# Optimization experiments

Measured on AMD Instinct MI355X. Metric: run time of the kernel, lower is better.

Reference implementation:

```python
import jax, jax.numpy as jnp
import numpy as np

N = 12288
E = 393216
IN_DIM = 128
HID = 64
QK = 32
K_HOPS = 2


def setup_inputs() -> dict:
    key = jax.random.key(0)
    ks = jax.random.split(key, 12)
    s = lambda k, shp, fan: jax.random.normal(k, shp, jnp.float32) / np.sqrt(fan)
    return {
        "x_train": jax.random.normal(ks[0], (N, IN_DIM), jnp.float32),
        "x_ori": jax.random.normal(ks[1], (N, IN_DIM), jnp.float32),
        "edge_index": jax.random.randint(ks[2], (2, E), 0, N, jnp.int64),
        "mask": jnp.zeros((N,), jnp.bool_),
        "W1": s(ks[3], (IN_DIM, HID), IN_DIM), "b1": jnp.zeros((HID,), jnp.float32),
        "W2": s(ks[4], (HID, HID), HID),      "b2": jnp.zeros((HID,), jnp.float32),
        "Wq": s(ks[5], (HID, QK), HID),       "bq": jnp.zeros((QK,), jnp.float32),
        "Wk": s(ks[6], (HID, QK), HID),       "bk": jnp.zeros((QK,), jnp.float32),
        "Wv": s(ks[7], (HID, HID), HID),      "bv": jnp.zeros((HID,), jnp.float32),
        "Wdx": s(ks[8], (HID, IN_DIM), HID),  "bdx": jnp.zeros((IN_DIM,), jnp.float32),
    }


def reference(x_train, x_ori, edge_index, mask,
              W1, b1, W2, b2, Wq, bq, Wk, bk, Wv, bv, Wdx, bdx):
    n = x_train.shape[0]
    row, col = edge_index[0], edge_index[1]

    # shared MLP: linear -> relu -> linear2 -> relu
    enc = lambda x: jax.nn.relu(jax.nn.relu(x @ W1 + b1) @ W2 + b2)
    h_ori = enc(x_ori)      # [N, HID]
    h_train = enc(x_train)  # [N, HID]

    # degree of source nodes, D^{-1/2}
    deg = jax.ops.segment_sum(jnp.ones_like(row, jnp.float32), row, num_segments=n)
    d_invsqrt = jnp.clip(deg, 1.0, None) ** -0.5  # [N]
    d_invsqrt = d_invsqrt[:, None]

    def lap(x):
        h = x * d_invsqrt
        out = jax.ops.segment_sum(h[row], col, num_segments=n)
        return x - out * d_invsqrt

    a_feat = 2.0 * h_train - lap(h_train)  # low-pass: 2I - L_sym
    stack = [a_feat]
    x = h_train
    for _ in range(K_HOPS):  # dropout inert in eval mode
        x = lap(x)
        stack.append(x)
    L = jnp.stack(stack, axis=1)  # [N, K+1, HID]

    # attention with global mean-pooled query over h_ori[~mask]
    w = (~mask).astype(jnp.float32)
    q_nodes = h_ori @ Wq + bq                              # [N, QK]
    q_global = (q_nodes * w[:, None]).sum(0) / jnp.clip(w.sum(), 1.0, None)  # [QK]
    keys = L @ Wk + bk   # [N, K+1, QK]
    vals = L @ Wv + bv   # [N, K+1, HID]
    scale = 1.0 / np.sqrt(HID)  # scale uses D = keys feature dim BEFORE projection
    scores = jnp.einsum('q,nkq->nk', q_global, keys) * scale
    A = jax.nn.softmax(scores, axis=-1)          # [N, K+1]
    z = jnp.einsum('nk,nkd->nd', A, vals)        # [N, HID]

    x_hat = z @ Wdx + bdx   # [N, IN_DIM]
    adj_hat = z @ z.T       # [N, N]
    return x_hat, adj_hat
```

## Files before the change

kernel.cpp:

```cpp
#include <hip/hip_runtime.h>
#include <hip/hip_bf16.h>

constexpr int N_  = 12288;
constexpr int E_  = 393216;
constexpr int IND = 128;
constexpr int HID = 64;
constexpr int QKD = 32;
constexpr int CAP = 96;

typedef __attribute__((ext_vector_type(4))) float f4raw;
typedef __attribute__((ext_vector_type(8))) __bf16 bf16x8;
typedef __attribute__((ext_vector_type(4))) __bf16 bf16x4;
typedef __attribute__((ext_vector_type(16))) float f32x16;

__device__ inline bf16x8 lds_read_bf8(const char* base, int row, int k) {
  int off = (row * 128 + k * 2) ^ ((row & 7) << 4);
  uint4 u = *(const uint4*)(base + off);
  union { uint4 u; bf16x8 v; } c; c.u = u; return c.v;
}
__device__ inline void lds_write_bf(char* base, int row, int col, __bf16 v) {
  int off = (row * 128 + col * 2) ^ ((row & 7) << 4);
  *(__bf16*)(base + off) = v;
}

__global__ __launch_bounds__(256) void prep_graph_kernel(
    const int* __restrict__ row, const int* __restrict__ col,
    const float* __restrict__ W1, const float* __restrict__ W2,
    const float* __restrict__ Wv, const float* __restrict__ Wdx,
    __bf16* __restrict__ W1T, __bf16* __restrict__ W2T,
    __bf16* __restrict__ WvT, __bf16* __restrict__ WdxT,
    int* degRow, int* cntCol, int* __restrict__ csrRow) {
  int b = blockIdx.x, tid = threadIdx.x;
  if (b < 384) {
    int e0 = (b * 256 + tid) * 4;
    int4 r4 = *(const int4*)(row + e0);
    atomicAdd(&degRow[r4.x], 1);
    atomicAdd(&degRow[r4.y], 1);
    atomicAdd(&degRow[r4.z], 1);
    atomicAdd(&degRow[r4.w], 1);
  } else if (b < 768) {
    int e0 = ((b - 384) * 256 + tid) * 4;
    int4 r4 = *(const int4*)(row + e0);
    int4 c4 = *(const int4*)(col + e0);
    int p;
    p = atomicAdd(&cntCol[c4.x], 1); csrRow[c4.x * CAP + p] = r4.x;
    p = atomicAdd(&cntCol[c4.y], 1); csrRow[c4.y * CAP + p] = r4.y;
    p = atomicAdd(&cntCol[c4.z], 1); csrRow[c4.z * CAP + p] = r4.z;
    p = atomicAdd(&cntCol[c4.w], 1); csrRow[c4.w * CAP + p] = r4.w;
  } else if (b == 768) {
    for (int e = tid; e < IND * HID; e += 256) {
      int c = e >> 7, k = e & 127;
      W1T[e] = (__bf16)W1[k * HID + c];
    }
  } else if (b == 769) {
    for (int e = tid; e < HID * HID; e += 256) {
      int c = e >> 6, k = e & 63;
      W2T[e] = (__bf16)W2[k * HID + c];
    }
  } else if (b == 770) {
    for (int e = tid; e < HID * HID; e += 256) {
      int c = e >> 6, k = e & 63;
      WvT[e] = (__bf16)Wv[k * HID + c];
    }
  } else {
    for (int e = tid; e < HID * IND; e += 256) {
      int c = e >> 6, k = e & 63;
      WdxT[e] = (__bf16)Wdx[k * IND + c];
    }
  }
}

__global__ __launch_bounds__(256) void enc_dinv_kernel(
    const float* __restrict__ xo, const float* __restrict__ xt,
    const __bf16* __restrict__ W1T, const float* __restrict__ b1,
    const __bf16* __restrict__ W2T, const float* __restrict__ b2,
    const int* __restrict__ degRow, const unsigned char* __restrict__ mask,
    float* __restrict__ h_tr, float* __restrict__ dinv, float* __restrict__ gsum) {
  __shared__ __align__(16) char h1s[2][32 * 128];
  __shared__ float wls[64];
  int b = blockIdx.x, tid = threadIdx.x;
  if (b >= 384) {
    int i0 = ((b - 384) * 256 + tid) * 4;
    int4 dg = *(const int4*)(degRow + i0);
    f4raw o = {rsqrtf((float)max(dg.x, 1)), rsqrtf((float)max(dg.y, 1)),
               rsqrtf((float)max(dg.z, 1)), rsqrtf((float)max(dg.w, 1))};
    *(f4raw*)(dinv + i0) = o;
    return;
  }
  bool ori = b < 192;
  int row0 = (ori ? b : b - 192) * 64;
  const float* xrow = (ori ? xo : xt) + (size_t)row0 * IND;
  if (ori && tid < 64) wls[tid] = mask[row0 + tid] ? 0.f : 1.f;
  int wave = tid >> 6, lane = tid & 63;
  int p = wave >> 1, w2 = wave & 1;
  int lr = lane & 31, hi = lane >> 5;
  int colc = w2 * 32 + lr;
  f32x16 acc = (f32x16)(0.f);
  const __bf16* wcol = W1T + (size_t)colc * IND + hi * 8;
  const float* arow = xrow + (size_t)(p * 32 + lr) * IND + hi * 8;
#pragma unroll
  for (int kk = 0; kk < 8; ++kk) {
    f4raw v0 = *(const f4raw*)(arow + kk * 16);
    f4raw v1 = *(const f4raw*)(arow + kk * 16 + 4);
    bf16x8 a;
    a[0] = (__bf16)v0.x; a[1] = (__bf16)v0.y; a[2] = (__bf16)v0.z; a[3] = (__bf16)v0.w;
    a[4] = (__bf16)v1.x; a[5] = (__bf16)v1.y; a[6] = (__bf16)v1.z; a[7] = (__bf16)v1.w;
    bf16x8 bq = *(const bf16x8*)(wcol + kk * 16);
    acc = __builtin_amdgcn_mfma_f32_32x32x16_bf16(a, bq, acc, 0, 0, 0);
  }
  float b1l = b1[colc];
#pragma unroll
  for (int reg = 0; reg < 16; ++reg) {
    int rr = (reg & 3) + 8 * (reg >> 2) + 4 * hi;
    float v = fmaxf(acc[reg] + b1l, 0.f);
    lds_write_bf(h1s[p], rr, colc, (__bf16)v);
  }
  __syncthreads();
  f32x16 acc2 = (f32x16)(0.f);
  const __bf16* wcol2 = W2T + (size_t)colc * HID + hi * 8;
#pragma unroll
  for (int kk = 0; kk < 4; ++kk) {
    bf16x8 a = lds_read_bf8(h1s[p], lr, kk * 16 + hi * 8);
    bf16x8 bq = *(const bf16x8*)(wcol2 + kk * 16);
    acc2 = __builtin_amdgcn_mfma_f32_32x32x16_bf16(a, bq, acc2, 0, 0, 0);
  }
  float b2l = b2[colc];
  if (ori) {
    float part = 0.f;
#pragma unroll
    for (int reg = 0; reg < 16; ++reg) {
      int rr = (reg & 3) + 8 * (reg >> 2) + 4 * hi;
      float v = fmaxf(acc2[reg] + b2l, 0.f);
      part = fmaf(wls[p * 32 + rr], v, part);
    }
    atomicAdd(&gsum[colc], part);
    if (tid == 0) {
      float wl = 0.f;
      for (int r = 0; r < 64; ++r) wl += wls[r];
      atomicAdd(&gsum[64], wl);
    }
  } else {
#pragma unroll
    for (int reg = 0; reg < 16; ++reg) {
      int rr = (reg & 3) + 8 * (reg >> 2) + 4 * hi;
      float v = fmaxf(acc2[reg] + b2l, 0.f);
      h_tr[(size_t)(row0 + p * 32 + rr) * HID + colc] = v;
    }
  }
}

__global__ __launch_bounds__(256) void lap1_kernel(
    const float* __restrict__ h, const float* __restrict__ dinv,
    const int* __restrict__ cnt, const int* __restrict__ csrRow,
    float* __restrict__ lap1d) {
  int lane = threadIdx.x & 63, wv = threadIdx.x >> 6;
  int g = lane >> 4, t = lane & 15;
  int c = blockIdx.x * 16 + wv * 4 + g;
  int s0 = c * CAP, s1 = s0 + cnt[c];
  f4raw a0 = (f4raw)(0.f), a1 = (f4raw)(0.f), a2 = (f4raw)(0.f), a3 = (f4raw)(0.f);
  int i = s0;
  for (; i + 3 < s1; i += 4) {
    int r0 = csrRow[i], r1 = csrRow[i + 1], r2 = csrRow[i + 2], r3 = csrRow[i + 3];
    a0 += (*(const f4raw*)(h + (size_t)r0 * HID + t * 4)) * dinv[r0];
    a1 += (*(const f4raw*)(h + (size_t)r1 * HID + t * 4)) * dinv[r1];
    a2 += (*(const f4raw*)(h + (size_t)r2 * HID + t * 4)) * dinv[r2];
    a3 += (*(const f4raw*)(h + (size_t)r3 * HID + t * 4)) * dinv[r3];
  }
  for (; i < s1; ++i) {
    int r0 = csrRow[i];
    a0 += (*(const f4raw*)(h + (size_t)r0 * HID + t * 4)) * dinv[r0];
  }
  float d = dinv[c];
  size_t idx = (size_t)c * HID + t * 4;
  f4raw hc = *(const f4raw*)(h + idx);
  *(f4raw*)(lap1d + idx) = (hc - ((a0 + a1) + (a2 + a3)) * d) * d;
}

__global__ __launch_bounds__(256) void lap2_attnz_xhat_kernel(
    const float* __restrict__ h, const float* __restrict__ lap1d,
    const float* __restrict__ dinv,
    const int* __restrict__ cnt, const int* __restrict__ csrRow,
    const float* __restrict__ gsum,
    const float* __restrict__ Wq, const float* __restrict__ bq,
    const float* __restrict__ Wk, const float* __restrict__ bk,
    const __bf16* __restrict__ WvT, const float* __restrict__ bv,
    const __bf16* __restrict__ WdxT, const float* __restrict__ bdx,
    float* __restrict__ xhat, __bf16* __restrict__ zb) {
  __shared__ float l2s[32][68];
  __shared__ __align__(16) char zps[32 * 128];
  __shared__ __align__(16) char zsl[32 * 128];
  __shared__ float qg[QKD];
  __shared__ float kqs[72];
  int tid = threadIdx.x;
  int row0 = blockIdx.x * 32;
  float wsum = gsum[64];
  if (tid < QKD) {
    float inv = 1.0f / fmaxf(wsum, 1.0f);
    float a = bq[tid] * wsum;
    for (int d0 = 0; d0 < HID; ++d0) a = fmaf(gsum[d0], Wq[d0 * QKD + tid], a);
    qg[tid] = a * inv;
  }
  int grp = tid >> 4, t = tid & 15;
#pragma unroll
  for (int it = 0; it < 2; ++it) {
    int r = grp + 16 * it;
    int c = row0 + r;
    int s0 = c * CAP, s1 = s0 + cnt[c];
    f4raw a0 = (f4raw)(0.f), a1 = (f4raw)(0.f), a2 = (f4raw)(0.f), a3 = (f4raw)(0.f);
    int i = s0;
    for (; i + 3 < s1; i += 4) {
      int r0 = csrRow[i], r1 = csrRow[i + 1], r2 = csrRow[i + 2], r3 = csrRow[i + 3];
      a0 += *(const f4raw*)(lap1d + (size_t)r0 * HID + t * 4);
      a1 += *(const f4raw*)(lap1d + (size_t)r1 * HID + t * 4);
      a2 += *(const f4raw*)(lap1d + (size_t)r2 * HID + t * 4);
      a3 += *(const f4raw*)(lap1d + (size_t)r3 * HID + t * 4);
    }
    for (; i < s1; ++i) {
      int r0 = csrRow[i];
      a0 += *(const f4raw*)(lap1d + (size_t)r0 * HID + t * 4);
    }
    float d = dinv[c];
    float rd = 1.0f / d;
    f4raw lv = *(const f4raw*)(lap1d + (size_t)c * HID + t * 4);
    *(f4raw*)&l2s[r][t * 4] = lv * rd - ((a0 + a1) + (a2 + a3)) * d;
  }
  __syncthreads();
  if (tid < 64) {
    float a = 0.f;
    for (int q = 0; q < QKD; ++q) a = fmaf(Wk[tid * QKD + q], qg[q], a);
    kqs[tid] = a * 0.125f;
  } else if (tid == 64) {
    float sb = 0.f;
    for (int q = 0; q < QKD; ++q) sb = fmaf(bk[q], qg[q], sb);
    kqs[64] = sb * 0.125f;
  }
  __syncthreads();
  f4raw kq4 = *(const f4raw*)(&kqs[t * 4]);
  float sbias = kqs[64];
#pragma unroll
  for (int it = 0; it < 2; ++it) {
    int r = grp + 16 * it;
    int c = row0 + r;
    size_t idx = (size_t)c * HID + t * 4;
    float d = dinv[c];
    float rd = 1.0f / d;
    f4raw hv = *(const f4raw*)(h + idx);
    f4raw v1 = *(const f4raw*)(lap1d + idx) * rd;
    f4raw v2 = *(const f4raw*)&l2s[r][t * 4];
    f4raw av = 2.f * hv - v1;
    float s0 = av.x * kq4.x + av.y * kq4.y + av.z * kq4.z + av.w * kq4.w;
    float s1 = v1.x * kq4.x + v1.y * kq4.y + v1.z * kq4.z + v1.w * kq4.w;
    float s2 = v2.x * kq4.x + v2.y * kq4.y + v2.z * kq4.z + v2.w * kq4.w;
#pragma unroll
    for (int o = 1; o < 16; o <<= 1) {
      s0 += __shfl_xor(s0, o);
      s1 += __shfl_xor(s1, o);
      s2 += __shfl_xor(s2, o);
    }
    s0 += sbias; s1 += sbias; s2 += sbias;
    float m = fmaxf(s0, fmaxf(s1, s2));
    float e0 = __expf(s0 - m), e1 = __expf(s1 - m), e2 = __expf(s2 - m);
    float is = 1.f / (e0 + e1 + e2);
    f4raw zp = (e0 * av + e1 * v1 + e2 * v2) * is;
    bf16x4 z4;
    z4[0] = (__bf16)zp.x; z4[1] = (__bf16)zp.y; z4[2] = (__bf16)zp.z; z4[3] = (__bf16)zp.w;
    int off = (r * 128 + t * 8) ^ ((r & 7) << 4);
    *(bf16x4*)(zps + off) = z4;
  }
  __syncthreads();
  int wave = tid >> 6, lane = tid & 63;
  int lr = lane & 31, hi = lane >> 5;
  if (wave < 2) {
    int col = wave * 32 + lr;
    f32x16 accz = (f32x16)(0.f);
    const __bf16* wv = WvT + (size_t)col * HID + hi * 8;
#pragma unroll
    for (int kk = 0; kk < 4; ++kk) {
      bf16x8 a = lds_read_bf8(zps, lr, kk * 16 + hi * 8);
      bf16x8 bq = *(const bf16x8*)(wv + kk * 16);
      accz = __builtin_amdgcn_mfma_f32_32x32x16_bf16(a, bq, accz, 0, 0, 0);
    }
    float bvl = bv[col];
#pragma unroll
    for (int reg = 0; reg < 16; ++reg) {
      int rr = (reg & 3) + 8 * (reg >> 2) + 4 * hi;
      __bf16 vb = (__bf16)(accz[reg] + bvl);
      zb[(size_t)(row0 + rr) * HID + col] = vb;
      lds_write_bf(zsl, rr, col, vb);
    }
  }
  __syncthreads();
  {
    int c0 = wave * 32 + lr;
    f32x16 acx = (f32x16)(0.f);
    const __bf16* wd = WdxT + (size_t)c0 * HID + hi * 8;
#pragma unroll
    for (int kk = 0; kk < 4; ++kk) {
      bf16x8 a = lds_read_bf8(zsl, lr, kk * 16 + hi * 8);
      bf16x8 bq = *(const bf16x8*)(wd + kk * 16);
      acx = __builtin_amdgcn_mfma_f32_32x32x16_bf16(a, bq, acx, 0, 0, 0);
    }
    float bdl = bdx[c0];
#pragma unroll
    for (int reg = 0; reg < 16; ++reg) {
      int rr = (reg & 3) + 8 * (reg >> 2) + 4 * hi;
      xhat[(size_t)(row0 + rr) * IND + c0] = acx[reg] + bdl;
    }
  }
}

__global__ __launch_bounds__(256) void adj_mfma_kernel(
    const __bf16* __restrict__ z, float* __restrict__ out) {
  int tid = threadIdx.x;
  int wave = tid >> 6, lane = tid & 63;
  int wr = wave >> 1, wc = wave & 1;
  int rb = blockIdx.y, cb = blockIdx.x;
  int lr = lane & 31, hi = lane >> 5;

  size_t arow0 = (size_t)(rb * 128 + wr * 64 + lr) * HID;
  size_t arow1 = arow0 + (size_t)32 * HID;
  size_t brow0 = (size_t)(cb * 128 + wc * 64 + lr) * HID;
  size_t brow1 = brow0 + (size_t)32 * HID;
  int kbase = hi * 8;

  f32x16 acc00 = (f32x16)(0.f), acc01 = (f32x16)(0.f);
  f32x16 acc10 = (f32x16)(0.f), acc11 = (f32x16)(0.f);

#pragma unroll
  for (int kk = 0; kk < 4; ++kk) {
    int k0 = kk * 16 + kbase;
    bf16x8 a0 = *(const bf16x8*)(z + arow0 + k0);
    bf16x8 a1 = *(const bf16x8*)(z + arow1 + k0);
    bf16x8 b0 = *(const bf16x8*)(z + brow0 + k0);
    bf16x8 b1 = *(const bf16x8*)(z + brow1 + k0);
    acc00 = __builtin_amdgcn_mfma_f32_32x32x16_bf16(a0, b0, acc00, 0, 0, 0);
    acc01 = __builtin_amdgcn_mfma_f32_32x32x16_bf16(a0, b1, acc01, 0, 0, 0);
    acc10 = __builtin_amdgcn_mfma_f32_32x32x16_bf16(a1, b0, acc10, 0, 0, 0);
    acc11 = __builtin_amdgcn_mfma_f32_32x32x16_bf16(a1, b1, acc11, 0, 0, 0);
  }

  int colb = cb * 128 + wc * 64 + lr;
  int rowb = rb * 128 + wr * 64 + 4 * hi;
#pragma unroll
  for (int reg = 0; reg < 16; ++reg) {
    int rr = (reg & 3) + 8 * (reg >> 2);
    size_t r0 = (size_t)(rowb + rr);
    __builtin_nontemporal_store(acc00[reg], out + r0 * N_ + colb);
    __builtin_nontemporal_store(acc01[reg], out + r0 * N_ + colb + 32);
    __builtin_nontemporal_store(acc10[reg], out + (r0 + 32) * N_ + colb);
    __builtin_nontemporal_store(acc11[reg], out + (r0 + 32) * N_ + colb + 32);
  }
}

extern "C" void kernel_launch(void* const* d_in, const int* in_sizes, int n_in,
                              void* d_out, int out_size, void* d_ws, size_t ws_size,
                              hipStream_t stream) {
  const float* x_train = (const float*)d_in[0];
  const float* x_ori   = (const float*)d_in[1];
  const int*   ei      = (const int*)d_in[2];
  const unsigned char* mask = (const unsigned char*)d_in[3];
  const float* W1  = (const float*)d_in[4];
  const float* b1  = (const float*)d_in[5];
  const float* W2  = (const float*)d_in[6];
  const float* b2  = (const float*)d_in[7];
  const float* Wq  = (const float*)d_in[8];
  const float* bq  = (const float*)d_in[9];
  const float* Wk  = (const float*)d_in[10];
  const float* bk  = (const float*)d_in[11];
  const float* Wv  = (const float*)d_in[12];
  const float* bv  = (const float*)d_in[13];
  const float* Wdx = (const float*)d_in[14];
  const float* bdx = (const float*)d_in[15];

  char* ws = (char*)d_ws;
  size_t o = 0;
  auto alloc = [&](size_t bytes) -> void* {
    void* p = ws + o;
    o += (bytes + 255) & ~(size_t)255;
    return p;
  };
  __bf16* W1T   = (__bf16*)alloc((size_t)IND * HID * 2);
  __bf16* W2T   = (__bf16*)alloc((size_t)HID * HID * 2);
  __bf16* WvT   = (__bf16*)alloc((size_t)HID * HID * 2);
  __bf16* WdxT  = (__bf16*)alloc((size_t)HID * IND * 2);
  float* h_tr   = (float*)alloc((size_t)N_ * HID * 4);
  float* lap1d  = (float*)alloc((size_t)N_ * HID * 4);
  __bf16* zb    = (__bf16*)alloc((size_t)N_ * HID * 2);
  float* dinv   = (float*)alloc((size_t)N_ * 4);
  int*   csrRow = (int*)alloc((size_t)N_ * CAP * 4);
  int*   zero0  = (int*)alloc((size_t)(2 * N_ + 65) * 4);
  int*   degRow = zero0;
  int*   cntCol = zero0 + N_;
  float* gsum   = (float*)(zero0 + 2 * N_);

  const int* row = ei;
  const int* col = ei + E_;

  (void)hipMemsetAsync(zero0, 0, (size_t)(2 * N_ + 65) * 4, stream);

  prep_graph_kernel<<<772, 256, 0, stream>>>(row, col, W1, W2, Wv, Wdx,
                                             W1T, W2T, WvT, WdxT,
                                             degRow, cntCol, csrRow);
  enc_dinv_kernel<<<396, 256, 0, stream>>>(x_ori, x_train, W1T, b1, W2T, b2,
                                           degRow, mask, h_tr, dinv, gsum);
  lap1_kernel<<<N_ / 16, 256, 0, stream>>>(h_tr, dinv, cntCol, csrRow, lap1d);

  float* outp = (float*)d_out;
  lap2_attnz_xhat_kernel<<<N_ / 32, 256, 0, stream>>>(h_tr, lap1d, dinv,
                                                      cntCol, csrRow, gsum,
                                                      Wq, bq, Wk, bk, WvT, bv,
                                                      WdxT, bdx, outp, zb);
  adj_mfma_kernel<<<dim3(96, 96), 256, 0, stream>>>(zb, outp + (size_t)N_ * IND);
}
```

Measured before the change: 247.8 us.

## Fuse graph prep and encoder into one kernel, compute dinv inside lap1

Merges the edge-counting/CSR-build kernel and the MLP encoder kernel into a single launch. Each encoder block now transposes W1/W2 into swizzled LDS itself instead of reading pre-transposed bf16 weights from global memory. The separate dinv pass is removed: lap1 computes rsqrt of degree on the fly for each neighbour and writes dinv for the later kernel. This saves a launch and a dependency, at the cost of redundant per-block weight staging, an extra LDS footprint that may lower occupancy, and repeated rsqrt work per edge.

```diff
diff --git a/kernel.cpp b/kernel.cpp
--- a/kernel.cpp
+++ b/kernel.cpp
@@ -22,14 +22,30 @@
   int off = (row * 128 + col * 2) ^ ((row & 7) << 4);
   *(__bf16*)(base + off) = v;
 }
-
-__global__ __launch_bounds__(256) void prep_graph_kernel(
+__device__ inline bf16x8 lds_read_bf8_256(const char* base, int row, int k) {
+  int off = (row * 256 + k * 2) ^ ((row & 7) << 4);
+  uint4 u = *(const uint4*)(base + off);
+  union { uint4 u; bf16x8 v; } c; c.u = u; return c.v;
+}
+__device__ inline void lds_write_bf_256(char* base, int row, int col, __bf16 v) {
+  int off = (row * 256 + col * 2) ^ ((row & 7) << 4);
+  *(__bf16*)(base + off) = v;
+}
+
+__global__ __launch_bounds__(256) void fused_front_kernel(
+    const float* __restrict__ xo, const float* __restrict__ xt,
     const int* __restrict__ row, const int* __restrict__ col,
-    const float* __restrict__ W1, const float* __restrict__ W2,
+    const float* __restrict__ W1, const float* __restrict__ b1,
+    const float* __restrict__ W2, const float* __restrict__ b2,
     const float* __restrict__ Wv, const float* __restrict__ Wdx,
-    __bf16* __restrict__ W1T, __bf16* __restrict__ W2T,
+    const unsigned char* __restrict__ mask,
     __bf16* __restrict__ WvT, __bf16* __restrict__ WdxT,
+    float* __restrict__ h_tr, float* __restrict__ gsum,
     int* degRow, int* cntCol, int* __restrict__ csrRow) {
+  __shared__ __align__(16) char W1s[16384];
+  __shared__ __align__(16) char W2s[8192];
+  __shared__ __align__(16) char h1s[2][4096];
+  __shared__ float wls[64];
   int b = blockIdx.x, tid = threadIdx.x;
   if (b < 384) {
     int e0 = (b * 256 + tid) * 4;
@@ -38,7 +54,9 @@
     atomicAdd(&degRow[r4.y], 1);
     atomicAdd(&degRow[r4.z], 1);
     atomicAdd(&degRow[r4.w], 1);
-  } else if (b < 768) {
+    return;
+  }
+  if (b < 768) {
     int e0 = ((b - 384) * 256 + tid) * 4;
     int4 r4 = *(const int4*)(row + e0);
     int4 c4 = *(const int4*)(col + e0);
@@ -47,56 +65,41 @@
     p = atomicAdd(&cntCol[c4.y], 1); csrRow[c4.y * CAP + p] = r4.y;
     p = atomicAdd(&cntCol[c4.z], 1); csrRow[c4.z * CAP + p] = r4.z;
     p = atomicAdd(&cntCol[c4.w], 1); csrRow[c4.w * CAP + p] = r4.w;
-  } else if (b == 768) {
-    for (int e = tid; e < IND * HID; e += 256) {
-      int c = e >> 7, k = e & 127;
-      W1T[e] = (__bf16)W1[k * HID + c];
-    }
-  } else if (b == 769) {
-    for (int e = tid; e < HID * HID; e += 256) {
-      int c = e >> 6, k = e & 63;
-      W2T[e] = (__bf16)W2[k * HID + c];
-    }
-  } else if (b == 770) {
+    return;
+  }
+  if (b == 768) {
     for (int e = tid; e < HID * HID; e += 256) {
       int c = e >> 6, k = e & 63;
       WvT[e] = (__bf16)Wv[k * HID + c];
     }
-  } else {
+    return;
+  }
+  if (b == 769) {
     for (int e = tid; e < HID * IND; e += 256) {
       int c = e >> 6, k = e & 63;
       WdxT[e] = (__bf16)Wdx[k * IND + c];
     }
-  }
-}
-
-__global__ __launch_bounds__(256) void enc_dinv_kernel(
-    const float* __restrict__ xo, const float* __restrict__ xt,
-    const __bf16* __restrict__ W1T, const float* __restrict__ b1,
-    const __bf16* __restrict__ W2T, const float* __restrict__ b2,
-    const int* __restrict__ degRow, const unsigned char* __restrict__ mask,
-    float* __restrict__ h_tr, float* __restrict__ dinv, float* __restrict__ gsum) {
-  __shared__ __align__(16) char h1s[2][32 * 128];
-  __shared__ float wls[64];
-  int b = blockIdx.x, tid = threadIdx.x;
-  if (b >= 384) {
-    int i0 = ((b - 384) * 256 + tid) * 4;
-    int4 dg = *(const int4*)(degRow + i0);
-    f4raw o = {rsqrtf((float)max(dg.x, 1)), rsqrtf((float)max(dg.y, 1)),
-               rsqrtf((float)max(dg.z, 1)), rsqrtf((float)max(dg.w, 1))};
-    *(f4raw*)(dinv + i0) = o;
     return;
   }
-  bool ori = b < 192;
-  int row0 = (ori ? b : b - 192) * 64;
+  int bb = b - 770;
+  bool ori = bb < 192;
+  int row0 = (ori ? bb : bb - 192) * 64;
   const float* xrow = (ori ? xo : xt) + (size_t)row0 * IND;
+  for (int e = tid; e < IND * HID; e += 256) {
+    int k = e >> 6, c = e & 63;
+    lds_write_bf_256(W1s, c, k, (__bf16)W1[e]);
+  }
+  for (int e = tid; e < HID * HID; e += 256) {
+    int k = e >> 6, c = e & 63;
+    lds_write_bf(W2s, c, k, (__bf16)W2[e]);
+  }
   if (ori && tid < 64) wls[tid] = mask[row0 + tid] ? 0.f : 1.f;
+  __syncthreads();
   int wave = tid >> 6, lane = tid & 63;
   int p = wave >> 1, w2 = wave & 1;
   int lr = lane & 31, hi = lane >> 5;
   int colc = w2 * 32 + lr;
   f32x16 acc = (f32x16)(0.f);
-  const __bf16* wcol = W1T + (size_t)colc * IND + hi * 8;
   const float* arow = xrow + (size_t)(p * 32 + lr) * IND + hi * 8;
 #pragma unroll
   for (int kk = 0; kk < 8; ++kk) {
@@ -105,7 +108,7 @@
     bf16x8 a;
     a[0] = (__bf16)v0.x; a[1] = (__bf16)v0.y; a[2] = (__bf16)v0.z; a[3] = (__bf16)v0.w;
     a[4] = (__bf16)v1.x; a[5] = (__bf16)v1.y; a[6] = (__bf16)v1.z; a[7] = (__bf16)v1.w;
-    bf16x8 bq = *(const bf16x8*)(wcol + kk * 16);
+    bf16x8 bq = lds_read_bf8_256(W1s, colc, kk * 16 + hi * 8);
     acc = __builtin_amdgcn_mfma_f32_32x32x16_bf16(a, bq, acc, 0, 0, 0);
   }
   float b1l = b1[colc];
@@ -117,11 +120,10 @@
   }
   __syncthreads();
   f32x16 acc2 = (f32x16)(0.f);
-  const __bf16* wcol2 = W2T + (size_t)colc * HID + hi * 8;
 #pragma unroll
   for (int kk = 0; kk < 4; ++kk) {
     bf16x8 a = lds_read_bf8(h1s[p], lr, kk * 16 + hi * 8);
-    bf16x8 bq = *(const bf16x8*)(wcol2 + kk * 16);
+    bf16x8 bq = lds_read_bf8(W2s, colc, kk * 16 + hi * 8);
     acc2 = __builtin_amdgcn_mfma_f32_32x32x16_bf16(a, bq, acc2, 0, 0, 0);
   }
   float b2l = b2[colc];
@@ -150,9 +152,9 @@
 }
 
 __global__ __launch_bounds__(256) void lap1_kernel(
-    const float* __restrict__ h, const float* __restrict__ dinv,
+    const float* __restrict__ h, const int* __restrict__ degRow,
     const int* __restrict__ cnt, const int* __restrict__ csrRow,
-    float* __restrict__ lap1d) {
+    float* __restrict__ lap1d, float* __restrict__ dinv) {
   int lane = threadIdx.x & 63, wv = threadIdx.x >> 6;
   int g = lane >> 4, t = lane & 15;
   int c = blockIdx.x * 16 + wv * 4 + g;
@@ -161,16 +163,22 @@
   int i = s0;
   for (; i + 3 < s1; i += 4) {
     int r0 = csrRow[i], r1 = csrRow[i + 1], r2 = csrRow[i + 2], r3 = csrRow[i + 3];
-    a0 += (*(const f4raw*)(h + (size_t)r0 * HID + t * 4)) * dinv[r0];
-    a1 += (*(const f4raw*)(h + (size_t)r1 * HID + t * 4)) * dinv[r1];
-    a2 += (*(const f4raw*)(h + (size_t)r2 * HID + t * 4)) * dinv[r2];
-    a3 += (*(const f4raw*)(h + (size_t)r3 * HID + t * 4)) * dinv[r3];
+    float d0 = rsqrtf((float)max(degRow[r0], 1));
+    float d1 = rsqrtf((float)max(degRow[r1], 1));
+    float d2 = rsqrtf((float)max(degRow[r2], 1));
+    float d3 = rsqrtf((float)max(degRow[r3], 1));
+    a0 += (*(const f4raw*)(h + (size_t)r0 * HID + t * 4)) * d0;
+    a1 += (*(const f4raw*)(h + (size_t)r1 * HID + t * 4)) * d1;
+    a2 += (*(const f4raw*)(h + (size_t)r2 * HID + t * 4)) * d2;
+    a3 += (*(const f4raw*)(h + (size_t)r3 * HID + t * 4)) * d3;
   }
   for (; i < s1; ++i) {
     int r0 = csrRow[i];
-    a0 += (*(const f4raw*)(h + (size_t)r0 * HID + t * 4)) * dinv[r0];
-  }
-  float d = dinv[c];
+    float d0 = rsqrtf((float)max(degRow[r0], 1));
+    a0 += (*(const f4raw*)(h + (size_t)r0 * HID + t * 4)) * d0;
+  }
+  float d = rsqrtf((float)max(degRow[c], 1));
+  if (t == 0) dinv[c] = d;
   size_t idx = (size_t)c * HID + t * 4;
   f4raw hc = *(const f4raw*)(h + idx);
   *(f4raw*)(lap1d + idx) = (hc - ((a0 + a1) + (a2 + a3)) * d) * d;
@@ -379,8 +387,6 @@
     o += (bytes + 255) & ~(size_t)255;
     return p;
   };
-  __bf16* W1T   = (__bf16*)alloc((size_t)IND * HID * 2);
-  __bf16* W2T   = (__bf16*)alloc((size_t)HID * HID * 2);
   __bf16* WvT   = (__bf16*)alloc((size_t)HID * HID * 2);
   __bf16* WdxT  = (__bf16*)alloc((size_t)HID * IND * 2);
   float* h_tr   = (float*)alloc((size_t)N_ * HID * 4);
@@ -398,12 +404,12 @@
 
   (void)hipMemsetAsync(zero0, 0, (size_t)(2 * N_ + 65) * 4, stream);
 
-  prep_graph_kernel<<<772, 256, 0, stream>>>(row, col, W1, W2, Wv, Wdx,
-                                             W1T, W2T, WvT, WdxT,
-                                             degRow, cntCol, csrRow);
-  enc_dinv_kernel<<<396, 256, 0, stream>>>(x_ori, x_train, W1T, b1, W2T, b2,
-                                           degRow, mask, h_tr, dinv, gsum);
-  lap1_kernel<<<N_ / 16, 256, 0, stream>>>(h_tr, dinv, cntCol, csrRow, lap1d);
+  fused_front_kernel<<<1154, 256, 0, stream>>>(x_ori, x_train, row, col,
+                                               W1, b1, W2, b2, Wv, Wdx, mask,
+                                               WvT, WdxT, h_tr, gsum,
+                                               degRow, cntCol, csrRow);
+  lap1_kernel<<<N_ / 16, 256, 0, stream>>>(h_tr, degRow, cntCol, csrRow,
+                                           lap1d, dinv);
 
   float* outp = (float*)d_out;
   lap2_attnz_xhat_kernel<<<N_ / 32, 256, 0, stream>>>(h_tr, lap1d, dinv,
```

Result: faster. 239.2 us (-3.5%).
